# Kernel tuning notes

Measured on AMD Instinct MI355X. Metric: run time of the kernel, lower is better.

Reference implementation:

```python
import jax, jax.numpy as jnp
import numpy as np

B, T, D, H, L, E, K = 4, 1024, 1024, 16, 2, 8, 2
HD = D // H                      # head_dim = 64
HALF = HD // 2                   # rope half dim = 32
CAP = int(np.ceil(2.0 * B * T / E))  # capacity factor 2 -> 1024
EPS = 1e-5


def build_sin_cos(seq_len, half_dim):
    pos = jnp.arange(seq_len, dtype=jnp.float32)[:, None]
    inv_freq = 1.0 / (10000.0 ** (jnp.arange(0, half_dim * 2, 2, dtype=jnp.float32) / (half_dim * 2)))
    ang = pos * inv_freq                      # (T, half_dim)
    return jnp.sin(ang), jnp.cos(ang)


def layernorm(x, g, b):
    mu = jnp.mean(x, -1, keepdims=True)
    var = jnp.mean(jnp.square(x - mu), -1, keepdims=True)
    return (x - mu) * jax.lax.rsqrt(var + EPS) * g + b


def attention(x, qkv_w, proj_w, sin, cos):
    # x: (B,T,D)
    qkv = (x @ qkv_w).reshape(B, T, H, 3 * HD)
    q, k, v = jnp.split(qkv, 3, axis=-1)      # each (B,T,H,HD)
    s = sin[None, :, None, :]                 # (1,T,1,HALF)
    c = cos[None, :, None, :]
    def rope(t):
        t1, t2 = t[..., :HALF], t[..., HALF:]
        return jnp.concatenate([t1 * c - t2 * s, t1 * s + t2 * c], axis=-1)
    q, k = rope(q), rope(k)
    scores = jnp.einsum('bqhd,bkhd->bhqk', q, k) / jnp.sqrt(jnp.float32(HD)).astype(x.dtype)
    causal = jnp.tril(jnp.ones((T, T), dtype=bool))
    scores = jnp.where(causal, scores, jnp.asarray(-1e9, scores.dtype))
    probs = jax.nn.softmax(scores, axis=-1)
    out = jnp.einsum('bhqk,bkhd->bqhd', probs, v).reshape(B, T, D)
    return out @ proj_w


def sparse_moe(x, gate_w, w1, b1, w2, b2):
    # eval mode: no router noise, aux_loss = 0
    flat = x.reshape(-1, D)                   # (N, D)
    N = flat.shape[0]
    gates = jax.nn.softmax((flat @ gate_w).astype(jnp.float32), axis=-1)  # (N, E)
    _, inds = jax.lax.top_k(gates, K)         # (N, K)
    mask = jnp.zeros((N, E), dtype=bool).at[jnp.arange(N)[:, None], inds].set(True)
    pos = jnp.cumsum(mask.astype(jnp.int32), axis=0) * mask - 1
    keep = (pos < CAP) & mask                 # (N, E) capacity-truncated assignment
    keepT = keep.T                            # (E, N)
    # stable argsort puts kept tokens first, preserving token order
    order = jnp.argsort(~keepT, axis=1)[:, :CAP]           # (E, CAP)
    valid = jnp.take_along_axis(keepT, order, axis=1)      # (E, CAP)
    safe = jnp.where(valid, order, 0)
    xg = flat[safe]                                        # (E, CAP, D)
    gv = jnp.take_along_axis(gates.T, safe, axis=1) * valid  # (E, CAP)
    h = jax.nn.gelu(jnp.einsum('ecd,edh->ech', xg, w1) + b1[:, None, :], approximate=False)
    out = jnp.einsum('ech,ehd->ecd', h, w2) + b2[:, None, :]
    contrib = out * gv[..., None].astype(flat.dtype)
    scatter_idx = jnp.where(valid, order, N)               # out-of-range -> dropped
    final = jnp.zeros_like(flat).at[scatter_idx.reshape(-1)].add(
        contrib.reshape(-1, D), mode='drop')
    return final.reshape(x.shape)


def setup_inputs() -> dict:
    key = jax.random.key(0)
    ks = jax.random.split(key, 8)
    s = 0.02
    return {
        'x': jax.random.normal(ks[0], (B, T, D), jnp.float32),
        'ln1_g': jnp.ones((L, D), jnp.float32),
        'ln1_b': jnp.zeros((L, D), jnp.float32),
        'qkv_w': jax.random.normal(ks[1], (L, D, 3 * D), jnp.float32) * s,
        'proj_w': jax.random.normal(ks[2], (L, D, D), jnp.float32) * s,
        'ln2_g': jnp.ones((L, D), jnp.float32),
        'ln2_b': jnp.zeros((L, D), jnp.float32),
        'gate_w': jax.random.normal(ks[3], (L, D, E), jnp.float32) * s,
        'w1': jax.random.normal(ks[4], (L, E, D, 4 * D), jnp.float32) * s,
        'b1': jnp.zeros((L, E, 4 * D), jnp.float32),
        'w2': jax.random.normal(ks[5], (L, E, 4 * D, D), jnp.float32) * s,
        'b2': jnp.zeros((L, E, D), jnp.float32),
    }


def reference(x, ln1_g, ln1_b, qkv_w, proj_w, ln2_g, ln2_b, gate_w, w1, b1, w2, b2):
    sin, cos = build_sin_cos(T, HALF)
    for l in range(L):
        x = x + attention(layernorm(x, ln1_g[l], ln1_b[l]), qkv_w[l], proj_w[l], sin, cos)
        x = x + sparse_moe(layernorm(x, ln2_g[l], ln2_b[l]), gate_w[l], w1[l], b1[l], w2[l], b2[l])
    return x
```

## Files before the change

kernel.cpp:

```cpp
#include <hip/hip_runtime.h>
#include <cstdint>

#define DD 1024
#define TT 1024
#define BB 4
#define HH 16
#define EE 8
#define NTOK 4096
#define CAPS 1024

using f16 = _Float16;
using f16x8 = __attribute__((ext_vector_type(8))) _Float16;
using f16x4 = __attribute__((ext_vector_type(4))) _Float16;
using f16x2 = __attribute__((ext_vector_type(2))) _Float16;
using f32x4 = __attribute__((ext_vector_type(4))) float;

#define MFMA16(a, b, c) __builtin_amdgcn_mfma_f32_16x16x32_f16(a, b, c, 0, 0, 0)

__device__ __forceinline__ void gload16(const void* g, void* l) {
  __builtin_amdgcn_global_load_lds((const __attribute__((address_space(1))) unsigned int*)g,
                                   (__attribute__((address_space(3))) unsigned int*)l, 16, 0, 0);
}

__device__ __forceinline__ void split2(float v, f16& h, f16& lo) {
  h = (f16)v;
  lo = (f16)((v - (float)h) * 2048.0f);
}

__device__ __forceinline__ void split_store(f16* ph, f16* pl, float v) {
  f16 h = (f16)v;
  *ph = h;
  *pl = (f16)((v - (float)h) * 2048.0f);
}

__launch_bounds__(256)
__global__ void splitT_k(const float* __restrict__ src, f16* __restrict__ dh, f16* __restrict__ dl,
                         int R, int C, long sSrc, long sDst) {
  __shared__ float tile[64][65];
  long z = blockIdx.z;
  src += z * sSrc; dh += z * sDst; dl += z * sDst;
  int c0 = blockIdx.x * 64, r0 = blockIdx.y * 64;
  int tid = threadIdx.x;
  int lrow = tid >> 2, lc = (tid & 3) * 16;
  const float* sp = src + (long)(r0 + lrow) * C + c0 + lc;
  #pragma unroll
  for (int j = 0; j < 4; ++j) {
    float4 v = *(const float4*)(sp + j * 4);
    tile[lrow][lc + j * 4 + 0] = v.x;
    tile[lrow][lc + j * 4 + 1] = v.y;
    tile[lrow][lc + j * 4 + 2] = v.z;
    tile[lrow][lc + j * 4 + 3] = v.w;
  }
  __syncthreads();
  int oc = tid >> 2, orr = (tid & 3) * 16;
  f16x8 h0, h1, l0, l1;
  #pragma unroll
  for (int j = 0; j < 8; ++j) {
    f16 h, lo;
    split2(tile[orr + j][oc], h, lo);
    h0[j] = h; l0[j] = lo;
    split2(tile[orr + 8 + j][oc], h, lo);
    h1[j] = h; l1[j] = lo;
  }
  long ob = (long)(c0 + oc) * R + r0 + orr;
  *(f16x8*)(dh + ob) = h0;
  *(f16x8*)(dh + ob + 8) = h1;
  *(f16x8*)(dl + ob) = l0;
  *(f16x8*)(dl + ob + 8) = l1;
}

template<bool GATE>
__launch_bounds__(256)
__global__ void ln_k(const float* __restrict__ x, const float* __restrict__ g, const float* __restrict__ b,
                     f16* __restrict__ oh, f16* __restrict__ ol,
                     const float* __restrict__ gw, float* __restrict__ gates) {
  int row = blockIdx.x, tid = threadIdx.x;
  int lane = tid & 63, wid = tid >> 6;
  __shared__ float red[4];
  __shared__ float pg[4][8];
  __shared__ float logits[8];
  const float* xr = x + (long)row * DD;
  int col = tid * 4;
  float4 v = *(const float4*)(xr + col);
  float s = v.x + v.y + v.z + v.w;
  #pragma unroll
  for (int off = 32; off >= 1; off >>= 1) s += __shfl_down(s, off);
  if (lane == 0) red[wid] = s;
  __syncthreads();
  float mu = (red[0] + red[1] + red[2] + red[3]) * (1.0f / DD);
  float d0 = v.x - mu, d1 = v.y - mu, d2 = v.z - mu, d3 = v.w - mu;
  float sq = d0 * d0 + d1 * d1 + d2 * d2 + d3 * d3;
  __syncthreads();
  #pragma unroll
  for (int off = 32; off >= 1; off >>= 1) sq += __shfl_down(sq, off);
  if (lane == 0) red[wid] = sq;
  __syncthreads();
  float var = (red[0] + red[1] + red[2] + red[3]) * (1.0f / DD);
  float rstd = rsqrtf(var + 1e-5f);
  float xv[4];
  xv[0] = d0 * rstd * g[col] + b[col];
  xv[1] = d1 * rstd * g[col + 1] + b[col + 1];
  xv[2] = d2 * rstd * g[col + 2] + b[col + 2];
  xv[3] = d3 * rstd * g[col + 3] + b[col + 3];
  f16x4 hv, lv;
  #pragma unroll
  for (int j = 0; j < 4; ++j) { f16 h, lo; split2(xv[j], h, lo); hv[j] = h; lv[j] = lo; }
  *(f16x4*)(oh + (long)row * DD + col) = hv;
  *(f16x4*)(ol + (long)row * DD + col) = lv;
  if (GATE) {
    float part[8];
    #pragma unroll
    for (int e = 0; e < 8; ++e) part[e] = 0.0f;
    #pragma unroll
    for (int j = 0; j < 4; ++j) {
      const float* gwr = gw + (long)(col + j) * 8;
      #pragma unroll
      for (int e = 0; e < 8; ++e) part[e] += xv[j] * gwr[e];
    }
    #pragma unroll
    for (int off = 32; off >= 1; off >>= 1) {
      #pragma unroll
      for (int e = 0; e < 8; ++e) part[e] += __shfl_down(part[e], off);
    }
    if (lane == 0) {
      #pragma unroll
      for (int e = 0; e < 8; ++e) pg[wid][e] = part[e];
    }
    __syncthreads();
    if (tid < 8) logits[tid] = pg[0][tid] + pg[1][tid] + pg[2][tid] + pg[3][tid];
    __syncthreads();
    if (tid < 8) {
      float mx = logits[0];
      #pragma unroll
      for (int e2 = 1; e2 < 8; ++e2) mx = fmaxf(mx, logits[e2]);
      float den = 0.0f;
      #pragma unroll
      for (int e2 = 0; e2 < 8; ++e2) den += expf(logits[e2] - mx);
      gates[(long)row * 8 + tid] = expf(logits[tid] - mx) / den;
    }
  }
}

__global__ void sincos_k(float* st, float* ct) {
  int i = blockIdx.x * 256 + threadIdx.x;
  if (i >= TT * 32) return;
  int t = i >> 5, f = i & 31;
  float inv = powf(10000.0f, -(float)f * (1.0f / 32.0f));
  float ang = (float)t * inv;
  st[i] = sinf(ang);
  ct[i] = cosf(ang);
}

__launch_bounds__(256, 2)
__global__ void attn_k(const f16* __restrict__ qh, const f16* __restrict__ ql,
                       const f16* __restrict__ kh, const f16* __restrict__ kl,
                       const f16* __restrict__ vth, const f16* __restrict__ vtl,
                       f16* __restrict__ oh_out, f16* __restrict__ ol_out) {
  __shared__ __align__(16) f16 KsH[4096], KsL[4096], VsH[4096], VsL[4096];
  __shared__ __align__(16) f16 Pw[4][2][2048];
  int bx = blockIdx.x;
  int bh = bx & 63;
  int qt = (int)((0x31204657u >> ((bx >> 6) << 2)) & 7u);
  int tid = threadIdx.x;
  int wid = tid >> 6, lane = tid & 63;
  int lr = lane & 15, lg = lane >> 4;
  long bhT = (long)bh * TT;
  int qrow0 = qt * 128 + wid * 32;
  int qend = qrow0 + 32;

  f16x8 qfh[2][2], qfl[2][2];
  #pragma unroll
  for (int qi = 0; qi < 2; ++qi) {
    long qoff = (bhT + qrow0 + qi * 16 + lr) * 64 + lg * 8;
    qfh[qi][0] = *(const f16x8*)(qh + qoff);
    qfh[qi][1] = *(const f16x8*)(qh + qoff + 32);
    qfl[qi][0] = *(const f16x8*)(ql + qoff);
    qfl[qi][1] = *(const f16x8*)(ql + qoff + 32);
  }

  f32x4 o_hi[2][4], o_md[2][4];
  #pragma unroll
  for (int qi = 0; qi < 2; ++qi)
    #pragma unroll
    for (int dj = 0; dj < 4; ++dj) {
      o_hi[qi][dj] = {0.f, 0.f, 0.f, 0.f};
      o_md[qi][dj] = {0.f, 0.f, 0.f, 0.f};
    }
  float m[2][4], lsum[2][4];
  #pragma unroll
  for (int qi = 0; qi < 2; ++qi)
    #pragma unroll
    for (int r = 0; r < 4; ++r) { m[qi][r] = -1e30f; lsum[qi][r] = 0.0f; }

  int srow = tid >> 3, slot = tid & 7;
  int gc = ((slot ^ (srow & 7)) << 3);
  const f16* kHp = kh + (bhT + srow) * 64 + gc;
  const f16* kLp = kl + (bhT + srow) * 64 + gc;
  const f16* vHp = vth + ((long)bh * 64 + srow) * TT + gc;
  const f16* vLp = vtl + ((long)bh * 64 + srow) * TT + gc;
  int t8 = tid * 8;
  int rsw = lr & 7;
  int c0 = ((lg ^ rsw) << 3), c1 = (((4 | lg) ^ rsw) << 3);
  f16* Ph = Pw[wid][0];
  f16* Pl = Pw[wid][1];

  int ntiles = 2 * (qt + 1);
  for (int kb = 0; kb < ntiles; ++kb) {
    int kv0 = kb * 64;
    gload16(kHp + (long)kv0 * 64, KsH + t8);
    gload16(kHp + (long)(kv0 + 32) * 64, KsH + 2048 + t8);
    gload16(kLp + (long)kv0 * 64, KsL + t8);
    gload16(kLp + (long)(kv0 + 32) * 64, KsL + 2048 + t8);
    gload16(vHp + kv0, VsH + t8);
    gload16(vHp + (long)32 * TT + kv0, VsH + 2048 + t8);
    gload16(vLp + kv0, VsL + t8);
    gload16(vLp + (long)32 * TT + kv0, VsL + 2048 + t8);
    __syncthreads();

    if (kv0 < qend) {
      f32x4 s[2][4];
      #pragma unroll
      for (int kj = 0; kj < 4; ++kj) {
        int rb = (kj * 16 + lr) * 64;
        f16x8 kfh0 = *(const f16x8*)(KsH + rb + c0);
        f16x8 kfh1 = *(const f16x8*)(KsH + rb + c1);
        f16x8 kfl0 = *(const f16x8*)(KsL + rb + c0);
        f16x8 kfl1 = *(const f16x8*)(KsL + rb + c1);
        #pragma unroll
        for (int qi = 0; qi < 2; ++qi) {
          f32x4 a = {0.f, 0.f, 0.f, 0.f};
          a = MFMA16(qfh[qi][0], kfh0, a);
          a = MFMA16(qfh[qi][1], kfh1, a);
          a = a * 2048.0f;
          a = MFMA16(qfh[qi][0], kfl0, a);
          a = MFMA16(qfh[qi][1], kfl1, a);
          a = MFMA16(qfl[qi][0], kfh0, a);
          a = MFMA16(qfl[qi][1], kfh1, a);
          s[qi][kj] = a;
        }
      }
      const float ss = 0.125f / 2048.0f;
      bool needmask = (kv0 + 64 > qrow0);
      float rm[2][4];
      #pragma unroll
      for (int qi = 0; qi < 2; ++qi)
        #pragma unroll
        for (int r = 0; r < 4; ++r) {
          int qrow = qrow0 + qi * 16 + lg * 4 + r;
          float mx = -1e30f;
          #pragma unroll
          for (int kj = 0; kj < 4; ++kj) {
            float v = s[qi][kj][r] * ss;
            if (needmask && (kv0 + kj * 16 + lr > qrow)) v = -1e9f;
            s[qi][kj][r] = v;
            mx = fmaxf(mx, v);
          }
          rm[qi][r] = mx;
        }
      #pragma unroll
      for (int off = 1; off < 16; off <<= 1)
        #pragma unroll
        for (int qi = 0; qi < 2; ++qi)
          #pragma unroll
          for (int r = 0; r < 4; ++r) rm[qi][r] = fmaxf(rm[qi][r], __shfl_xor(rm[qi][r], off));
      float alpha[2][4], rs[2][4];
      #pragma unroll
      for (int qi = 0; qi < 2; ++qi)
        #pragma unroll
        for (int r = 0; r < 4; ++r) {
          float mn = fmaxf(m[qi][r], rm[qi][r]);
          alpha[qi][r] = __expf(m[qi][r] - mn);
          m[qi][r] = mn;
          rs[qi][r] = 0.0f;
        }
      #pragma unroll
      for (int qi = 0; qi < 2; ++qi)
        #pragma unroll
        for (int kj = 0; kj < 4; ++kj)
          #pragma unroll
          for (int r = 0; r < 4; ++r) {
            float p = __expf(s[qi][kj][r] - m[qi][r]);
            rs[qi][r] += p;
            int prow = qi * 16 + lg * 4 + r;
            int pcol = kj * 16 + lr;
            int idx = prow * 64 + (((pcol >> 3) ^ (prow & 7)) << 3) + (pcol & 7);
            f16 hv = (f16)p;
            Ph[idx] = hv;
            Pl[idx] = (f16)((p - (float)hv) * 2048.0f);
          }
      #pragma unroll
      for (int off = 1; off < 16; off <<= 1)
        #pragma unroll
        for (int qi = 0; qi < 2; ++qi)
          #pragma unroll
          for (int r = 0; r < 4; ++r) rs[qi][r] += __shfl_xor(rs[qi][r], off);
      #pragma unroll
      for (int qi = 0; qi < 2; ++qi)
        #pragma unroll
        for (int r = 0; r < 4; ++r) lsum[qi][r] = lsum[qi][r] * alpha[qi][r] + rs[qi][r];
      #pragma unroll
      for (int qi = 0; qi < 2; ++qi)
        #pragma unroll
        for (int dj = 0; dj < 4; ++dj)
          #pragma unroll
          for (int r = 0; r < 4; ++r) {
            o_hi[qi][dj][r] *= alpha[qi][r];
            o_md[qi][dj][r] *= alpha[qi][r];
          }
      f16x8 pah[2][2], pal[2][2];
      #pragma unroll
      for (int qi = 0; qi < 2; ++qi) {
        int pr = (qi * 16 + lr) * 64;
        pah[qi][0] = *(const f16x8*)(Ph + pr + c0);
        pah[qi][1] = *(const f16x8*)(Ph + pr + c1);
        pal[qi][0] = *(const f16x8*)(Pl + pr + c0);
        pal[qi][1] = *(const f16x8*)(Pl + pr + c1);
      }
      #pragma unroll
      for (int dj = 0; dj < 4; ++dj) {
        int vb = (dj * 16 + lr) * 64;
        f16x8 vh0 = *(const f16x8*)(VsH + vb + c0);
        f16x8 vh1 = *(const f16x8*)(VsH + vb + c1);
        f16x8 vl0 = *(const f16x8*)(VsL + vb + c0);
        f16x8 vl1 = *(const f16x8*)(VsL + vb + c1);
        #pragma unroll
        for (int qi = 0; qi < 2; ++qi) {
          o_hi[qi][dj] = MFMA16(pah[qi][0], vh0, o_hi[qi][dj]);
          o_hi[qi][dj] = MFMA16(pah[qi][1], vh1, o_hi[qi][dj]);
          o_md[qi][dj] = MFMA16(pah[qi][0], vl0, o_md[qi][dj]);
          o_md[qi][dj] = MFMA16(pah[qi][1], vl1, o_md[qi][dj]);
          o_md[qi][dj] = MFMA16(pal[qi][0], vh0, o_md[qi][dj]);
          o_md[qi][dj] = MFMA16(pal[qi][1], vh1, o_md[qi][dj]);
        }
      }
    }
    __syncthreads();
  }

  int b = bh >> 4, hh = bh & 15;
  #pragma unroll
  for (int qi = 0; qi < 2; ++qi)
    #pragma unroll
    for (int r = 0; r < 4; ++r) {
      float invl = 1.0f / lsum[qi][r];
      int qrow = qrow0 + qi * 16 + lg * 4 + r;
      long obase = ((long)(b * TT + qrow)) * DD + hh * 64 + lr;
      #pragma unroll
      for (int dj = 0; dj < 4; ++dj) {
        float val = (o_hi[qi][dj][r] + o_md[qi][dj][r] * (1.0f / 2048.0f)) * invl;
        f16 hv = (f16)val;
        oh_out[obase + dj * 16] = hv;
        ol_out[obase + dj * 16] = (f16)((val - (float)hv) * 2048.0f);
      }
    }
}

template<int EPI, bool SPLIT>
__launch_bounds__(256, 2)
__global__ void gemmF(const f16* __restrict__ Ah, const f16* __restrict__ Al, long sA,
                      const f16* __restrict__ Bh, const f16* __restrict__ Bl, long sB,
                      int M, int N, int K, int smode,
                      float* __restrict__ outF, long sOutF,
                      const float* __restrict__ resid,
                      const float* __restrict__ bias, long sBias,
                      f16* __restrict__ outH, f16* __restrict__ outL, long sOutH,
                      f16* __restrict__ q4h, f16* __restrict__ q4l,
                      f16* __restrict__ k4h, f16* __restrict__ k4l) {
  __shared__ __align__(16) f16 pool[(SPLIT ? 4 : 2) * 128 * 64];
  f16* AsH = pool;
  f16* BsH = pool + 8192;
  f16* AsL = SPLIT ? pool + 16384 : pool;
  f16* BsL = SPLIT ? pool + 24576 : pool;

  int bm, bn, z;
  if (smode == 0) {
    bn = blockIdx.x; bm = blockIdx.y; z = blockIdx.z;
  } else {
    int id = blockIdx.x;
    int logical;
    if (smode == 1) { z = id & 7; logical = id >> 3; }
    else { z = 0; int cpx = (int)(gridDim.x >> 3); logical = (id & 7) * cpx + (id >> 3); }
    int st = logical >> 6, wi = logical & 63;
    int nstm = (smode == 1) ? 1 : (M >> 10);
    int stm = st % nstm, stn = st / nstm;
    bm = (stm << 3) | (wi & 7);
    bn = (stn << 3) | (wi >> 3);
  }

  int tid = threadIdx.x;
  int wid = tid >> 6, lane = tid & 63;
  int wm = (wid >> 1) * 64, wn = (wid & 1) * 64;
  int lr = lane & 15, lg = lane >> 4;

  f32x4 aH[4][4], aL[4][4];
  #pragma unroll
  for (int i = 0; i < 4; ++i)
    #pragma unroll
    for (int j = 0; j < 4; ++j) {
      aH[i][j] = {0.f, 0.f, 0.f, 0.f};
      if (SPLIT) aL[i][j] = {0.f, 0.f, 0.f, 0.f};
    }

  int srow = tid >> 3;
  int gcol = (((tid & 7) ^ (srow & 7)) << 3);
  const f16* apH = Ah + (long)z * sA + ((long)(bm * 128 + srow)) * K + gcol;
  const f16* bpH = Bh + (long)z * sB + ((long)(bn * 128 + srow)) * K + gcol;
  const f16* apL = nullptr; const f16* bpL = nullptr;
  if (SPLIT) {
    apL = Al + (long)z * sA + ((long)(bm * 128 + srow)) * K + gcol;
    bpL = Bl + (long)z * sB + ((long)(bn * 128 + srow)) * K + gcol;
  }
  int tid8 = tid * 8;
  int rsw = lr & 7;

  for (int kt = 0; kt < K; kt += 64) {
    #pragma unroll
    for (int r4 = 0; r4 < 4; ++r4) {
      long go = (long)kt + (long)(r4 * 32) * K;
      int lo = tid8 + r4 * 2048;
      gload16(apH + go, AsH + lo);
      gload16(bpH + go, BsH + lo);
      if (SPLIT) {
        gload16(apL + go, AsL + lo);
        gload16(bpL + go, BsL + lo);
      }
    }
    __syncthreads();
    #pragma unroll
    for (int kk2 = 0; kk2 < 2; ++kk2) {
      int sws = (((kk2 << 2) | lg) ^ rsw) << 3;
      f16x8 afH[4], afL[4];
      #pragma unroll
      for (int i = 0; i < 4; ++i) {
        int ro = (wm + i * 16 + lr) * 64 + sws;
        afH[i] = *(const f16x8*)(AsH + ro);
        if (SPLIT) afL[i] = *(const f16x8*)(AsL + ro);
      }
      #pragma unroll
      for (int j = 0; j < 4; ++j) {
        int ro = (wn + j * 16 + lr) * 64 + sws;
        f16x8 bH = *(const f16x8*)(BsH + ro);
        #pragma unroll
        for (int i = 0; i < 4; ++i) aH[i][j] = MFMA16(afH[i], bH, aH[i][j]);
        if (SPLIT) {
          f16x8 bL = *(const f16x8*)(BsL + ro);
          #pragma unroll
          for (int i = 0; i < 4; ++i) {
            aL[i][j] = MFMA16(afH[i], bL, aL[i][j]);
            aL[i][j] = MFMA16(afL[i], bH, aL[i][j]);
          }
        }
      }
    }
    __syncthreads();
  }

  if (EPI == 4) {
    int c64 = (bn * 128 + wn) >> 6;
    int type = c64 % 3, hd = c64 / 3;
    const float* stab = resid;
    const float* ctab = bias;
    #pragma unroll
    for (int i = 0; i < 4; ++i) {
      #pragma unroll
      for (int r = 0; r < 4; ++r) {
        int row = bm * 128 + wm + i * 16 + lg * 4 + r;
        int b = row >> 10, t = row & (TT - 1);
        long bh = (long)(b * HH + hd);
        if (type == 2) {
          #pragma unroll
          for (int j = 0; j < 4; ++j) {
            float v = aH[i][j][r] + aL[i][j][r] * (1.0f / 2048.0f);
            int d = j * 16 + lr;
            long idx = (bh * 64 + d) * TT + t;
            split_store(outH + idx, outL + idx, v);
          }
        } else {
          f16* oh = (type == 0) ? q4h : k4h;
          f16* ol = (type == 0) ? q4l : k4l;
          long obase = (bh * TT + t) * 64;
          #pragma unroll
          for (int j = 0; j < 2; ++j) {
            int half = j * 16 + lr;
            float sa = stab[t * 32 + half], ca = ctab[t * 32 + half];
            float x1 = aH[i][j][r] + aL[i][j][r] * (1.0f / 2048.0f);
            float x2 = aH[i][j + 2][r] + aL[i][j + 2][r] * (1.0f / 2048.0f);
            split_store(oh + obase + half, ol + obase + half, x1 * ca - x2 * sa);
            split_store(oh + obase + half + 32, ol + obase + half + 32, x1 * sa + x2 * ca);
          }
        }
      }
    }
    return;
  }

  #pragma unroll
  for (int i = 0; i < 4; ++i) {
    #pragma unroll
    for (int j = 0; j < 4; ++j) {
      #pragma unroll
      for (int r = 0; r < 4; ++r) {
        int row = bm * 128 + wm + i * 16 + lg * 4 + r;
        int col = bn * 128 + wn + j * 16 + lr;
        float v = aH[i][j][r];
        if (SPLIT) v += aL[i][j][r] * (1.0f / 2048.0f);
        if (EPI == 0) {
          outF[(long)row * N + col] = v;
        } else if (EPI == 1) {
          long idx = (long)row * N + col;
          outF[idx] = v + resid[idx];
        } else if (EPI == 2) {
          float t = v + bias[(long)z * sBias + col];
          float ge = 0.5f * t * (1.0f + erff(t * 0.70710678118f));
          long idx = (long)z * sOutH + (long)row * N + col;
          f16 hv = (f16)ge;
          outH[idx] = hv;
          if (SPLIT) outL[idx] = (f16)((ge - (float)hv) * 2048.0f);
        } else {
          long idx = (long)z * sOutF + (long)row * N + col;
          outF[idx] = v + bias[(long)z * sBias + col];
        }
      }
    }
  }
}

__launch_bounds__(512)
__global__ void route_k(const float* __restrict__ gates, int* __restrict__ etok, int* __restrict__ slotof) {
  __shared__ unsigned char lmask[NTOK];
  __shared__ unsigned char ltop[NTOK];
  int tid = threadIdx.x;
  for (int t = tid; t < NTOK; t += 512) {
    const float* gr = gates + (long)t * 8;
    float gv[8];
    #pragma unroll
    for (int e = 0; e < 8; ++e) gv[e] = gr[e];
    int e1 = 0; float bv = gv[0];
    #pragma unroll
    for (int e = 1; e < 8; ++e) if (gv[e] > bv) { bv = gv[e]; e1 = e; }
    int e2 = -1; float bv2 = -1e30f;
    #pragma unroll
    for (int e = 0; e < 8; ++e) if (e != e1 && gv[e] > bv2) { bv2 = gv[e]; e2 = e; }
    lmask[t] = (unsigned char)((1u << e1) | (1u << e2));
    ltop[t] = (unsigned char)(e1 | (e2 << 4));
    slotof[t * 2] = -1;
    slotof[t * 2 + 1] = -1;
  }
  __syncthreads();
  int e = tid >> 6, lane = tid & 63;
  int cnt = 0;
  for (int c = 0; c < NTOK / 64; ++c) {
    int t = c * 64 + lane;
    int bit = (lmask[t] >> e) & 1;
    unsigned long long bal = __ballot(bit);
    int pre = __popcll(bal & ((1ull << lane) - 1ull));
    int slot = cnt + pre;
    if (bit && slot < CAPS) {
      etok[e * CAPS + slot] = t;
      int tp = ltop[t];
      int k = ((tp & 15) == e) ? 0 : 1;
      slotof[t * 2 + k] = (e << 16) | slot;
    }
    cnt += __popcll(bal);
  }
  int kept = cnt < CAPS ? cnt : CAPS;
  for (int s = kept + lane; s < CAPS; s += 64) etok[e * CAPS + s] = 0;
}

__global__ void gather_k(const int* __restrict__ etok, const f16* __restrict__ xh, const f16* __restrict__ xl,
                         f16* __restrict__ gh, f16* __restrict__ gl) {
  int es = blockIdx.x, tid = threadIdx.x;
  int tok = etok[es];
  const uint4* s1 = (const uint4*)(xh + (long)tok * DD);
  const uint4* s2 = (const uint4*)(xl + (long)tok * DD);
  ((uint4*)(gh + (long)es * DD))[tid] = s1[tid];
  ((uint4*)(gl + (long)es * DD))[tid] = s2[tid];
}

__global__ void scatter_k(const int* __restrict__ slotof, const float* __restrict__ gates,
                          const float* __restrict__ moe, float* __restrict__ x) {
  int t = blockIdx.x, tid = threadIdx.x;
  int s0 = slotof[t * 2], s1 = slotof[t * 2 + 1];
  float4* xr = (float4*)(x + (long)t * DD);
  float4 v = xr[tid];
  if (s0 >= 0) {
    int e = s0 >> 16, sl = s0 & 0xffff;
    float gv = gates[(long)t * 8 + e];
    float4 mo = ((const float4*)(moe + ((long)e * CAPS + sl) * DD))[tid];
    v.x += gv * mo.x; v.y += gv * mo.y; v.z += gv * mo.z; v.w += gv * mo.w;
  }
  if (s1 >= 0) {
    int e = s1 >> 16, sl = s1 & 0xffff;
    float gv = gates[(long)t * 8 + e];
    float4 mo = ((const float4*)(moe + ((long)e * CAPS + sl) * DD))[tid];
    v.x += gv * mo.x; v.y += gv * mo.y; v.z += gv * mo.z; v.w += gv * mo.w;
  }
  xr[tid] = v;
}

extern "C" void kernel_launch(void* const* d_in, const int* in_sizes, int n_in,
                              void* d_out, int out_size, void* d_ws, size_t ws_size,
                              hipStream_t stream) {
  const float* x_in   = (const float*)d_in[0];
  const float* ln1_g  = (const float*)d_in[1];
  const float* ln1_b  = (const float*)d_in[2];
  const float* qkv_w  = (const float*)d_in[3];
  const float* proj_w = (const float*)d_in[4];
  const float* ln2_g  = (const float*)d_in[5];
  const float* ln2_b  = (const float*)d_in[6];
  const float* gate_w = (const float*)d_in[7];
  const float* w1     = (const float*)d_in[8];
  const float* b1     = (const float*)d_in[9];
  const float* w2     = (const float*)d_in[10];
  const float* b2     = (const float*)d_in[11];
  float* x = (float*)d_out;

  char* p = (char*)d_ws;
  auto alloc = [&](size_t bytes) { char* r = p; p += (bytes + 255) & ~(size_t)255; return (void*)r; };

  f16* Wreg   = (f16*)alloc(134217728);
  f16* qhB  = (f16*)alloc(4194304ull * 2);
  f16* qlB  = (f16*)alloc(4194304ull * 2);
  f16* khB  = (f16*)alloc(4194304ull * 2);
  f16* klB  = (f16*)alloc(4194304ull * 2);
  f16* vthB = (f16*)alloc(4194304ull * 2);
  f16* vtlB = (f16*)alloc(4194304ull * 2);
  f16* xnh  = (f16*)alloc(4194304ull * 2);
  f16* xnl  = (f16*)alloc(4194304ull * 2);
  f16* atth = (f16*)alloc(4194304ull * 2);
  f16* attl = (f16*)alloc(4194304ull * 2);
  f16* xgh  = (f16*)alloc(8388608ull * 2);
  f16* xgl  = (f16*)alloc(8388608ull * 2);
  f16* hhB  = (f16*)alloc(33554432ull * 2);
  f16* hlB  = (f16*)alloc(33554432ull * 2);
  float* moe = (float*)alloc(8388608ull * 4);
  float* stab = (float*)alloc(32768ull * 4);
  float* ctab = (float*)alloc(32768ull * 4);
  float* gates = (float*)alloc(32768ull * 4);
  int* etok  = (int*)alloc(8192ull * 4);
  int* slotof = (int*)alloc(8192ull * 4);

  f16* qkvTh = Wreg;
  f16* qkvTl = Wreg + 3145728;
  f16* projTh = Wreg + 2 * 3145728;
  f16* projTl = Wreg + 2 * 3145728 + 1048576;
  f16* w1Th = Wreg;
  f16* w1Tl = Wreg + 33554432;
  f16* w2Th = Wreg;
  f16* w2Tl = Wreg + 33554432;

  hipMemcpyAsync(x, x_in, (size_t)NTOK * DD * 4, hipMemcpyDeviceToDevice, stream);
  sincos_k<<<(TT * 32 + 255) / 256, 256, 0, stream>>>(stab, ctab);

  for (int l = 0; l < 2; ++l) {
    splitT_k<<<dim3(3072 / 64, 1024 / 64, 1), 256, 0, stream>>>(
        qkv_w + (long)l * DD * 3072, qkvTh, qkvTl, 1024, 3072, 0, 0);
    splitT_k<<<dim3(1024 / 64, 1024 / 64, 1), 256, 0, stream>>>(
        proj_w + (long)l * DD * DD, projTh, projTl, 1024, 1024, 0, 0);
    ln_k<false><<<NTOK, 256, 0, stream>>>(x, ln1_g + l * DD, ln1_b + l * DD, xnh, xnl, nullptr, nullptr);
    gemmF<4, true><<<768, 256, 0, stream>>>(
        xnh, xnl, 0, qkvTh, qkvTl, 0, 4096, 3072, 1024, 2,
        nullptr, 0, stab, ctab, 0, vthB, vtlB, 0, qhB, qlB, khB, klB);
    attn_k<<<512, 256, 0, stream>>>(qhB, qlB, khB, klB, vthB, vtlB, atth, attl);
    gemmF<1, true><<<256, 256, 0, stream>>>(
        atth, attl, 0, projTh, projTl, 0, 4096, 1024, 1024, 2,
        x, 0, x, nullptr, 0, nullptr, nullptr, 0, nullptr, nullptr, nullptr, nullptr);

    ln_k<true><<<NTOK, 256, 0, stream>>>(x, ln2_g + l * DD, ln2_b + l * DD, xnh, xnl,
                                         gate_w + (long)l * DD * EE, gates);
    route_k<<<1, 512, 0, stream>>>(gates, etok, slotof);
    gather_k<<<EE * CAPS, 128, 0, stream>>>(etok, xnh, xnl, xgh, xgl);
    splitT_k<<<dim3(4096 / 64, 1024 / 64, EE), 256, 0, stream>>>(
        w1 + (long)l * EE * DD * 4096, w1Th, w1Tl, 1024, 4096, (long)DD * 4096, (long)4096 * DD);
    if (l == 0) {
      gemmF<2, true><<<2048, 256, 0, stream>>>(
          xgh, xgl, (long)CAPS * DD, w1Th, w1Tl, (long)4096 * DD, 1024, 4096, 1024, 1,
          nullptr, 0, nullptr, b1 + (long)l * EE * 4096, 4096, hhB, hlB, (long)CAPS * 4096,
          nullptr, nullptr, nullptr, nullptr);
    } else {
      gemmF<2, false><<<2048, 256, 0, stream>>>(
          xgh, xgl, (long)CAPS * DD, w1Th, w1Tl, (long)4096 * DD, 1024, 4096, 1024, 1,
          nullptr, 0, nullptr, b1 + (long)l * EE * 4096, 4096, hhB, hlB, (long)CAPS * 4096,
          nullptr, nullptr, nullptr, nullptr);
    }
    splitT_k<<<dim3(1024 / 64, 4096 / 64, EE), 256, 0, stream>>>(
        w2 + (long)l * EE * 4096 * DD, w2Th, w2Tl, 4096, 1024, (long)4096 * DD, (long)DD * 4096);
    if (l == 0) {
      gemmF<3, true><<<512, 256, 0, stream>>>(
          hhB, hlB, (long)CAPS * 4096, w2Th, w2Tl, (long)DD * 4096, 1024, 1024, 4096, 1,
          moe, (long)CAPS * DD, nullptr, b2 + (long)l * EE * DD, DD, nullptr, nullptr, 0,
          nullptr, nullptr, nullptr, nullptr);
    } else {
      gemmF<3, false><<<512, 256, 0, stream>>>(
          hhB, hlB, (long)CAPS * 4096, w2Th, w2Tl, (long)DD * 4096, 1024, 1024, 4096, 1,
          moe, (long)CAPS * DD, nullptr, b2 + (long)l * EE * DD, DD, nullptr, nullptr, 0,
          nullptr, nullptr, nullptr, nullptr);
    }
    scatter_k<<<NTOK, 256, 0, stream>>>(slotof, gates, moe, x);
  }
  (void)in_sizes; (void)n_in; (void)out_size; (void)ws_size;
}
```

Measured before the change: 1.461 ms.

## Read attention K/V straight from global memory and skip unused low weight halves

The attention kernel no longer stages K and V tiles through shared memory with block-wide barriers. Each wave now loads its K/V fragments directly from global memory and loops only over the key tiles its own query rows need. The occupancy hint rises to three blocks per CU now that the shared footprint is smaller. The weight split kernel gains a template flag so layer-1 MoE weights skip computing and storing the low-precision halves, since the gemmF<...,false> path for that layer appears not to read them. The trade is redundant global/L2 traffic across the four waves in place of LDS reuse, plus possible register pressure under the tighter launch bound.

```diff
diff --git a/kernel.cpp b/kernel.cpp
--- a/kernel.cpp
+++ b/kernel.cpp
@@ -12,7 +12,6 @@
 using f16 = _Float16;
 using f16x8 = __attribute__((ext_vector_type(8))) _Float16;
 using f16x4 = __attribute__((ext_vector_type(4))) _Float16;
-using f16x2 = __attribute__((ext_vector_type(2))) _Float16;
 using f32x4 = __attribute__((ext_vector_type(4))) float;
 
 #define MFMA16(a, b, c) __builtin_amdgcn_mfma_f32_16x16x32_f16(a, b, c, 0, 0, 0)
@@ -33,6 +32,7 @@
   *pl = (f16)((v - (float)h) * 2048.0f);
 }
 
+template<bool LO>
 __launch_bounds__(256)
 __global__ void splitT_k(const float* __restrict__ src, f16* __restrict__ dh, f16* __restrict__ dl,
                          int R, int C, long sSrc, long sDst) {
@@ -56,17 +56,20 @@
   f16x8 h0, h1, l0, l1;
   #pragma unroll
   for (int j = 0; j < 8; ++j) {
-    f16 h, lo;
-    split2(tile[orr + j][oc], h, lo);
-    h0[j] = h; l0[j] = lo;
-    split2(tile[orr + 8 + j][oc], h, lo);
-    h1[j] = h; l1[j] = lo;
+    float v0 = tile[orr + j][oc], v1 = tile[orr + 8 + j][oc];
+    h0[j] = (f16)v0; h1[j] = (f16)v1;
+    if (LO) {
+      l0[j] = (f16)((v0 - (float)h0[j]) * 2048.0f);
+      l1[j] = (f16)((v1 - (float)h1[j]) * 2048.0f);
+    }
   }
   long ob = (long)(c0 + oc) * R + r0 + orr;
   *(f16x8*)(dh + ob) = h0;
   *(f16x8*)(dh + ob + 8) = h1;
-  *(f16x8*)(dl + ob) = l0;
-  *(f16x8*)(dl + ob + 8) = l1;
+  if (LO) {
+    *(f16x8*)(dl + ob) = l0;
+    *(f16x8*)(dl + ob + 8) = l1;
+  }
 }
 
 template<bool GATE>
@@ -151,12 +154,11 @@
   ct[i] = cosf(ang);
 }
 
-__launch_bounds__(256, 2)
+__launch_bounds__(256, 3)
 __global__ void attn_k(const f16* __restrict__ qh, const f16* __restrict__ ql,
                        const f16* __restrict__ kh, const f16* __restrict__ kl,
                        const f16* __restrict__ vth, const f16* __restrict__ vtl,
                        f16* __restrict__ oh_out, f16* __restrict__ ol_out) {
-  __shared__ __align__(16) f16 KsH[4096], KsL[4096], VsH[4096], VsL[4096];
   __shared__ __align__(16) f16 Pw[4][2][2048];
   int bx = blockIdx.x;
   int bh = bx & 63;
@@ -192,149 +194,134 @@
     #pragma unroll
     for (int r = 0; r < 4; ++r) { m[qi][r] = -1e30f; lsum[qi][r] = 0.0f; }
 
-  int srow = tid >> 3, slot = tid & 7;
-  int gc = ((slot ^ (srow & 7)) << 3);
-  const f16* kHp = kh + (bhT + srow) * 64 + gc;
-  const f16* kLp = kl + (bhT + srow) * 64 + gc;
-  const f16* vHp = vth + ((long)bh * 64 + srow) * TT + gc;
-  const f16* vLp = vtl + ((long)bh * 64 + srow) * TT + gc;
-  int t8 = tid * 8;
   int rsw = lr & 7;
   int c0 = ((lg ^ rsw) << 3), c1 = (((4 | lg) ^ rsw) << 3);
   f16* Ph = Pw[wid][0];
   f16* Pl = Pw[wid][1];
 
-  int ntiles = 2 * (qt + 1);
-  for (int kb = 0; kb < ntiles; ++kb) {
+  const f16* kbh = kh + bhT * 64;
+  const f16* kbl = kl + bhT * 64;
+  const f16* vbh = vth + (long)bh * 64 * TT;
+  const f16* vbl = vtl + (long)bh * 64 * TT;
+
+  int ntw = (qend + 63) >> 6;
+  for (int kb = 0; kb < ntw; ++kb) {
     int kv0 = kb * 64;
-    gload16(kHp + (long)kv0 * 64, KsH + t8);
-    gload16(kHp + (long)(kv0 + 32) * 64, KsH + 2048 + t8);
-    gload16(kLp + (long)kv0 * 64, KsL + t8);
-    gload16(kLp + (long)(kv0 + 32) * 64, KsL + 2048 + t8);
-    gload16(vHp + kv0, VsH + t8);
-    gload16(vHp + (long)32 * TT + kv0, VsH + 2048 + t8);
-    gload16(vLp + kv0, VsL + t8);
-    gload16(vLp + (long)32 * TT + kv0, VsL + 2048 + t8);
-    __syncthreads();
-
-    if (kv0 < qend) {
-      f32x4 s[2][4];
-      #pragma unroll
-      for (int kj = 0; kj < 4; ++kj) {
-        int rb = (kj * 16 + lr) * 64;
-        f16x8 kfh0 = *(const f16x8*)(KsH + rb + c0);
-        f16x8 kfh1 = *(const f16x8*)(KsH + rb + c1);
-        f16x8 kfl0 = *(const f16x8*)(KsL + rb + c0);
-        f16x8 kfl1 = *(const f16x8*)(KsL + rb + c1);
+    f32x4 s[2][4];
+    #pragma unroll
+    for (int kj = 0; kj < 4; ++kj) {
+      long ko = (long)(kv0 + kj * 16 + lr) * 64 + lg * 8;
+      f16x8 kfh0 = *(const f16x8*)(kbh + ko);
+      f16x8 kfh1 = *(const f16x8*)(kbh + ko + 32);
+      f16x8 kfl0 = *(const f16x8*)(kbl + ko);
+      f16x8 kfl1 = *(const f16x8*)(kbl + ko + 32);
+      #pragma unroll
+      for (int qi = 0; qi < 2; ++qi) {
+        f32x4 a = {0.f, 0.f, 0.f, 0.f};
+        a = MFMA16(qfh[qi][0], kfh0, a);
+        a = MFMA16(qfh[qi][1], kfh1, a);
+        a = a * 2048.0f;
+        a = MFMA16(qfh[qi][0], kfl0, a);
+        a = MFMA16(qfh[qi][1], kfl1, a);
+        a = MFMA16(qfl[qi][0], kfh0, a);
+        a = MFMA16(qfl[qi][1], kfh1, a);
+        s[qi][kj] = a;
+      }
+    }
+    const float ss = 0.125f / 2048.0f;
+    bool needmask = (kv0 + 64 > qrow0);
+    float rm[2][4];
+    #pragma unroll
+    for (int qi = 0; qi < 2; ++qi)
+      #pragma unroll
+      for (int r = 0; r < 4; ++r) {
+        int qrow = qrow0 + qi * 16 + lg * 4 + r;
+        float mx = -1e30f;
         #pragma unroll
-        for (int qi = 0; qi < 2; ++qi) {
-          f32x4 a = {0.f, 0.f, 0.f, 0.f};
-          a = MFMA16(qfh[qi][0], kfh0, a);
-          a = MFMA16(qfh[qi][1], kfh1, a);
-          a = a * 2048.0f;
-          a = MFMA16(qfh[qi][0], kfl0, a);
-          a = MFMA16(qfh[qi][1], kfl1, a);
-          a = MFMA16(qfl[qi][0], kfh0, a);
-          a = MFMA16(qfl[qi][1], kfh1, a);
-          s[qi][kj] = a;
+        for (int kj = 0; kj < 4; ++kj) {
+          float v = s[qi][kj][r] * ss;
+          if (needmask && (kv0 + kj * 16 + lr > qrow)) v = -1e9f;
+          s[qi][kj][r] = v;
+          mx = fmaxf(mx, v);
         }
-      }
-      const float ss = 0.125f / 2048.0f;
-      bool needmask = (kv0 + 64 > qrow0);
-      float rm[2][4];
+        rm[qi][r] = mx;
+      }
+    #pragma unroll
+    for (int off = 1; off < 16; off <<= 1)
       #pragma unroll
       for (int qi = 0; qi < 2; ++qi)
         #pragma unroll
+        for (int r = 0; r < 4; ++r) rm[qi][r] = fmaxf(rm[qi][r], __shfl_xor(rm[qi][r], off));
+    float alpha[2][4], rs[2][4];
+    #pragma unroll
+    for (int qi = 0; qi < 2; ++qi)
+      #pragma unroll
+      for (int r = 0; r < 4; ++r) {
+        float mn = fmaxf(m[qi][r], rm[qi][r]);
+        alpha[qi][r] = __expf(m[qi][r] - mn);
+        m[qi][r] = mn;
+        rs[qi][r] = 0.0f;
+      }
+    #pragma unroll
+    for (int qi = 0; qi < 2; ++qi)
+      #pragma unroll
+      for (int kj = 0; kj < 4; ++kj)
+        #pragma unroll
         for (int r = 0; r < 4; ++r) {
-          int qrow = qrow0 + qi * 16 + lg * 4 + r;
-          float mx = -1e30f;
-          #pragma unroll
-          for (int kj = 0; kj < 4; ++kj) {
-            float v = s[qi][kj][r] * ss;
-            if (needmask && (kv0 + kj * 16 + lr > qrow)) v = -1e9f;
-            s[qi][kj][r] = v;
-            mx = fmaxf(mx, v);
-          }
-          rm[qi][r] = mx;
+          float p = __expf(s[qi][kj][r] - m[qi][r]);
+          rs[qi][r] += p;
+          int prow = qi * 16 + lg * 4 + r;
+          int pcol = kj * 16 + lr;
+          int idx = prow * 64 + (((pcol >> 3) ^ (prow & 7)) << 3) + (pcol & 7);
+          f16 hv = (f16)p;
+          Ph[idx] = hv;
+          Pl[idx] = (f16)((p - (float)hv) * 2048.0f);
         }
-      #pragma unroll
-      for (int off = 1; off < 16; off <<= 1)
-        #pragma unroll
-        for (int qi = 0; qi < 2; ++qi)
-          #pragma unroll
-          for (int r = 0; r < 4; ++r) rm[qi][r] = fmaxf(rm[qi][r], __shfl_xor(rm[qi][r], off));
-      float alpha[2][4], rs[2][4];
+    #pragma unroll
+    for (int off = 1; off < 16; off <<= 1)
       #pragma unroll
       for (int qi = 0; qi < 2; ++qi)
         #pragma unroll
+        for (int r = 0; r < 4; ++r) rs[qi][r] += __shfl_xor(rs[qi][r], off);
+    #pragma unroll
+    for (int qi = 0; qi < 2; ++qi)
+      #pragma unroll
+      for (int r = 0; r < 4; ++r) lsum[qi][r] = lsum[qi][r] * alpha[qi][r] + rs[qi][r];
+    #pragma unroll
+    for (int qi = 0; qi < 2; ++qi)
+      #pragma unroll
+      for (int dj = 0; dj < 4; ++dj)
+        #pragma unroll
         for (int r = 0; r < 4; ++r) {
-          float mn = fmaxf(m[qi][r], rm[qi][r]);
-          alpha[qi][r] = __expf(m[qi][r] - mn);
-          m[qi][r] = mn;
-          rs[qi][r] = 0.0f;
+          o_hi[qi][dj][r] *= alpha[qi][r];
+          o_md[qi][dj][r] *= alpha[qi][r];
         }
-      #pragma unroll
-      for (int qi = 0; qi < 2; ++qi)
-        #pragma unroll
-        for (int kj = 0; kj < 4; ++kj)
-          #pragma unroll
-          for (int r = 0; r < 4; ++r) {
-            float p = __expf(s[qi][kj][r] - m[qi][r]);
-            rs[qi][r] += p;
-            int prow = qi * 16 + lg * 4 + r;
-            int pcol = kj * 16 + lr;
-            int idx = prow * 64 + (((pcol >> 3) ^ (prow & 7)) << 3) + (pcol & 7);
-            f16 hv = (f16)p;
-            Ph[idx] = hv;
-            Pl[idx] = (f16)((p - (float)hv) * 2048.0f);
-          }
-      #pragma unroll
-      for (int off = 1; off < 16; off <<= 1)
-        #pragma unroll
-        for (int qi = 0; qi < 2; ++qi)
-          #pragma unroll
-          for (int r = 0; r < 4; ++r) rs[qi][r] += __shfl_xor(rs[qi][r], off);
-      #pragma unroll
-      for (int qi = 0; qi < 2; ++qi)
-        #pragma unroll
-        for (int r = 0; r < 4; ++r) lsum[qi][r] = lsum[qi][r] * alpha[qi][r] + rs[qi][r];
-      #pragma unroll
-      for (int qi = 0; qi < 2; ++qi)
-        #pragma unroll
-        for (int dj = 0; dj < 4; ++dj)
-          #pragma unroll
-          for (int r = 0; r < 4; ++r) {
-            o_hi[qi][dj][r] *= alpha[qi][r];
-            o_md[qi][dj][r] *= alpha[qi][r];
-          }
-      f16x8 pah[2][2], pal[2][2];
+    f16x8 pah[2][2], pal[2][2];
+    #pragma unroll
+    for (int qi = 0; qi < 2; ++qi) {
+      int pr = (qi * 16 + lr) * 64;
+      pah[qi][0] = *(const f16x8*)(Ph + pr + c0);
+      pah[qi][1] = *(const f16x8*)(Ph + pr + c1);
+      pal[qi][0] = *(const f16x8*)(Pl + pr + c0);
+      pal[qi][1] = *(const f16x8*)(Pl + pr + c1);
+    }
+    #pragma unroll
+    for (int dj = 0; dj < 4; ++dj) {
+      long vo = (long)(dj * 16 + lr) * TT + kv0 + lg * 8;
+      f16x8 vh0 = *(const f16x8*)(vbh + vo);
+      f16x8 vh1 = *(const f16x8*)(vbh + vo + 32);
+      f16x8 vl0 = *(const f16x8*)(vbl + vo);
+      f16x8 vl1 = *(const f16x8*)(vbl + vo + 32);
       #pragma unroll
       for (int qi = 0; qi < 2; ++qi) {
-        int pr = (qi * 16 + lr) * 64;
-        pah[qi][0] = *(const f16x8*)(Ph + pr + c0);
-        pah[qi][1] = *(const f16x8*)(Ph + pr + c1);
-        pal[qi][0] = *(const f16x8*)(Pl + pr + c0);
-        pal[qi][1] = *(const f16x8*)(Pl + pr + c1);
-      }
-      #pragma unroll
-      for (int dj = 0; dj < 4; ++dj) {
-        int vb = (dj * 16 + lr) * 64;
-        f16x8 vh0 = *(const f16x8*)(VsH + vb + c0);
-        f16x8 vh1 = *(const f16x8*)(VsH + vb + c1);
-        f16x8 vl0 = *(const f16x8*)(VsL + vb + c0);
-        f16x8 vl1 = *(const f16x8*)(VsL + vb + c1);
-        #pragma unroll
-        for (int qi = 0; qi < 2; ++qi) {
-          o_hi[qi][dj] = MFMA16(pah[qi][0], vh0, o_hi[qi][dj]);
-          o_hi[qi][dj] = MFMA16(pah[qi][1], vh1, o_hi[qi][dj]);
-          o_md[qi][dj] = MFMA16(pah[qi][0], vl0, o_md[qi][dj]);
-          o_md[qi][dj] = MFMA16(pah[qi][1], vl1, o_md[qi][dj]);
-          o_md[qi][dj] = MFMA16(pal[qi][0], vh0, o_md[qi][dj]);
-          o_md[qi][dj] = MFMA16(pal[qi][1], vh1, o_md[qi][dj]);
-        }
-      }
-    }
-    __syncthreads();
+        o_hi[qi][dj] = MFMA16(pah[qi][0], vh0, o_hi[qi][dj]);
+        o_hi[qi][dj] = MFMA16(pah[qi][1], vh1, o_hi[qi][dj]);
+        o_md[qi][dj] = MFMA16(pah[qi][0], vl0, o_md[qi][dj]);
+        o_md[qi][dj] = MFMA16(pah[qi][1], vl1, o_md[qi][dj]);
+        o_md[qi][dj] = MFMA16(pal[qi][0], vh0, o_md[qi][dj]);
+        o_md[qi][dj] = MFMA16(pal[qi][1], vh1, o_md[qi][dj]);
+      }
+    }
   }
 
   int b = bh >> 4, hh = bh & 15;
@@ -653,9 +640,9 @@
   sincos_k<<<(TT * 32 + 255) / 256, 256, 0, stream>>>(stab, ctab);
 
   for (int l = 0; l < 2; ++l) {
-    splitT_k<<<dim3(3072 / 64, 1024 / 64, 1), 256, 0, stream>>>(
+    splitT_k<true><<<dim3(3072 / 64, 1024 / 64, 1), 256, 0, stream>>>(
         qkv_w + (long)l * DD * 3072, qkvTh, qkvTl, 1024, 3072, 0, 0);
-    splitT_k<<<dim3(1024 / 64, 1024 / 64, 1), 256, 0, stream>>>(
+    splitT_k<true><<<dim3(1024 / 64, 1024 / 64, 1), 256, 0, stream>>>(
         proj_w + (long)l * DD * DD, projTh, projTl, 1024, 1024, 0, 0);
     ln_k<false><<<NTOK, 256, 0, stream>>>(x, ln1_g + l * DD, ln1_b + l * DD, xnh, xnl, nullptr, nullptr);
     gemmF<4, true><<<768, 256, 0, stream>>>(
@@ -670,27 +657,28 @@
                                          gate_w + (long)l * DD * EE, gates);
     route_k<<<1, 512, 0, stream>>>(gates, etok, slotof);
     gather_k<<<EE * CAPS, 128, 0, stream>>>(etok, xnh, xnl, xgh, xgl);
-    splitT_k<<<dim3(4096 / 64, 1024 / 64, EE), 256, 0, stream>>>(
-        w1 + (long)l * EE * DD * 4096, w1Th, w1Tl, 1024, 4096, (long)DD * 4096, (long)4096 * DD);
     if (l == 0) {
+      splitT_k<true><<<dim3(4096 / 64, 1024 / 64, EE), 256, 0, stream>>>(
+          w1 + (long)l * EE * DD * 4096, w1Th, w1Tl, 1024, 4096, (long)DD * 4096, (long)4096 * DD);
       gemmF<2, true><<<2048, 256, 0, stream>>>(
           xgh, xgl, (long)CAPS * DD, w1Th, w1Tl, (long)4096 * DD, 1024, 4096, 1024, 1,
           nullptr, 0, nullptr, b1 + (long)l * EE * 4096, 4096, hhB, hlB, (long)CAPS * 4096,
           nullptr, nullptr, nullptr, nullptr);
-    } else {
-      gemmF<2, false><<<2048, 256, 0, stream>>>(
-          xgh, xgl, (long)CAPS * DD, w1Th, w1Tl, (long)4096 * DD, 1024, 4096, 1024, 1,
-          nullptr, 0, nullptr, b1 + (long)l * EE * 4096, 4096, hhB, hlB, (long)CAPS * 4096,
-          nullptr, nullptr, nullptr, nullptr);
-    }
-    splitT_k<<<dim3(1024 / 64, 4096 / 64, EE), 256, 0, stream>>>(
-        w2 + (long)l * EE * 4096 * DD, w2Th, w2Tl, 4096, 1024, (long)4096 * DD, (long)DD * 4096);
-    if (l == 0) {
+      splitT_k<true><<<dim3(1024 / 64, 4096 / 64, EE), 256, 0, stream>>>(
+          w2 + (long)l * EE * 4096 * DD, w2Th, w2Tl, 4096, 1024, (long)4096 * DD, (long)DD * 4096);
       gemmF<3, true><<<512, 256, 0, stream>>>(
           hhB, hlB, (long)CAPS * 4096, w2Th, w2Tl, (long)DD * 4096, 1024, 1024, 4096, 1,
           moe, (long)CAPS * DD, nullptr, b2 + (long)l * EE * DD, DD, nullptr, nullptr, 0,
           nullptr, nullptr, nullptr, nullptr);
     } else {
+      splitT_k<false><<<dim3(4096 / 64, 1024 / 64, EE), 256, 0, stream>>>(
+          w1 + (long)l * EE * DD * 4096, w1Th, w1Tl, 1024, 4096, (long)DD * 4096, (long)4096 * DD);
+      gemmF<2, false><<<2048, 256, 0, stream>>>(
+          xgh, xgl, (long)CAPS * DD, w1Th, w1Tl, (long)4096 * DD, 1024, 4096, 1024, 1,
+          nullptr, 0, nullptr, b1 + (long)l * EE * 4096, 4096, hhB, hlB, (long)CAPS * 4096,
+          nullptr, nullptr, nullptr, nullptr);
+      splitT_k<false><<<dim3(1024 / 64, 4096 / 64, EE), 256, 0, stream>>>(
+          w2 + (long)l * EE * 4096 * DD, w2Th, w2Tl, 4096, 1024, (long)4096 * DD, (long)DD * 4096);
       gemmF<3, false><<<512, 256, 0, stream>>>(
           hhB, hlB, (long)CAPS * 4096, w2Th, w2Tl, (long)DD * 4096, 1024, 1024, 4096, 1,
           moe, (long)CAPS * DD, nullptr, b2 + (long)l * EE * DD, DD, nullptr, nullptr, 0,
```

After: 1.755 ms. 1.2x slower.
